# Optimization experiments

Hardware: AMD Instinct MI355X
Metric: run time of the kernel (lower is better)

The kernel has to match this reference:

```python
import jax, jax.numpy as jnp
import numpy as np

N_NODES = 1_000_000
N_EDGES = 16_000_000


def setup_inputs() -> dict:
    key = jax.random.key(0)
    k = jax.random.split(key, 6)
    x = jax.random.normal(k[0], (N_NODES, 1), dtype=jnp.float32)
    edge_index = jax.random.randint(k[1], (2, N_EDGES), 0, N_NODES, dtype=jnp.int32)
    W1 = jax.random.normal(k[2], (1, 16), dtype=jnp.float32) * (1.0 / np.sqrt(1))
    b1 = jnp.zeros((16,), dtype=jnp.float32)
    W2 = jax.random.normal(k[3], (16, 2), dtype=jnp.float32) * (1.0 / np.sqrt(16))
    b2 = jnp.zeros((2,), dtype=jnp.float32)
    return {"x": x, "edge_index": edge_index, "W1": W1, "b1": b1, "W2": W2, "b2": b2}


def _gcn_norm(edge_index, num_nodes):
    # PyG GCNConv default: add self-loops, symmetric normalization.
    loops = jnp.arange(num_nodes, dtype=edge_index.dtype)
    row = jnp.concatenate([edge_index[0], loops])  # source
    col = jnp.concatenate([edge_index[1], loops])  # target
    deg = jax.ops.segment_sum(jnp.ones_like(col, dtype=jnp.float32), col,
                              num_segments=num_nodes)
    dis = jnp.where(deg > 0, jax.lax.rsqrt(jnp.maximum(deg, 1.0)), 0.0)
    norm = dis[row] * dis[col]  # [E + N]
    return row, col, norm


def _gcn_conv(x, row, col, norm, W, b, num_nodes):
    h = x @ W                                   # [N, out]
    msg = h[row] * norm[:, None]                # gather + scale per edge
    out = jax.ops.segment_sum(msg, col, num_segments=num_nodes)
    return out + b


def reference(x, edge_index, W1, b1, W2, b2):
    n = x.shape[0]
    row, col, norm = _gcn_norm(edge_index, n)
    h = jax.nn.relu(_gcn_conv(x, row, col, norm, W1, b1, n))
    out = _gcn_conv(h, row, col, norm, W2, b2, n)
    return jax.nn.log_softmax(out, axis=1)
```

## Files before the change

kernel.cpp:

```cpp
#include <hip/hip_runtime.h>
#include <hip/hip_fp16.h>


namespace {

constexpr int N_NODES = 1000000;
constexpr int BUCKET_SHIFT = 11;
constexpr int NPB = 1 << BUCKET_SHIFT;
constexpr int NBUCKET = (N_NODES + NPB - 1) / NPB;
constexpr int CHUNK = 32768;
constexpr int NP = 512;
constexpr int TB = 1024;
constexpr int BATCH = 4096;

static_assert(NBUCKET <= 512, "wave scan assumes <=512 buckets");

typedef int intv4 __attribute__((ext_vector_type(4)));
typedef float floatv2 __attribute__((ext_vector_type(2)));

__device__ inline intv4 ntload4(const int* p) {
  return __builtin_nontemporal_load((const intv4*)p);
}
__device__ inline unsigned ntloadu(const unsigned* p) {
  return __builtin_nontemporal_load(p);
}

__device__ inline void wave_scan_512(const unsigned* arr, unsigned* outp, int n,
                                     unsigned* tot) {
  int lane = threadIdx.x;
  unsigned v[8];
  unsigned s = 0;
  int base8 = lane * 8;
#pragma unroll
  for (int k = 0; k < 8; ++k) {
    unsigned xv = (base8 + k < n) ? arr[base8 + k] : 0u;
    v[k] = s; s += xv;
  }
  unsigned run = s;
#pragma unroll
  for (int d = 1; d < 64; d <<= 1) {
    unsigned o = __shfl_up(run, d, 64);
    if (lane >= d) run += o;
  }
  unsigned excl = run - s;
#pragma unroll
  for (int k = 0; k < 8; ++k)
    if (base8 + k < n) outp[base8 + k] = excl + v[k];
  if (lane == 63 && tot) *tot = excl + s;
}


__global__ void k_hist(const int* __restrict__ col, int E,
                       unsigned* __restrict__ H) {
  __shared__ unsigned hist[NBUCKET];
  for (int i = threadIdx.x; i < NBUCKET; i += TB) hist[i] = 0u;
  __syncthreads();
  const int c = blockIdx.x;
  const int cbase = c * CHUNK;
  const int cend = min(cbase + CHUNK, E);
  for (int i0 = cbase + threadIdx.x * 4; i0 < cend; i0 += TB * 4) {
    if (i0 + 4 <= cend) {
      intv4 cc = ntload4(col + i0);
      atomicAdd(&hist[((unsigned)cc.x) >> BUCKET_SHIFT], 1u);
      atomicAdd(&hist[((unsigned)cc.y) >> BUCKET_SHIFT], 1u);
      atomicAdd(&hist[((unsigned)cc.z) >> BUCKET_SHIFT], 1u);
      atomicAdd(&hist[((unsigned)cc.w) >> BUCKET_SHIFT], 1u);
    } else {
      for (int i = i0; i < cend; ++i)
        atomicAdd(&hist[((unsigned)col[i]) >> BUCKET_SHIFT], 1u);
    }
  }
  __syncthreads();
  for (int b = threadIdx.x; b < NBUCKET; b += TB)
    H[(size_t)b * NP + c] = hist[b];
}

__global__ void k_scan1(unsigned* __restrict__ H, int nchunk,
                        unsigned* __restrict__ total) {
  unsigned* Hrow = H + (size_t)blockIdx.x * NP;
  wave_scan_512(Hrow, Hrow, nchunk, total + blockIdx.x);
}

__global__ void k_scan2(const unsigned* __restrict__ total,
                        unsigned* __restrict__ ebase) {
  wave_scan_512(total, ebase, NBUCKET, nullptr);
}

__global__ void k_bin(const int* __restrict__ row, const int* __restrict__ col,
                      int E, const unsigned* __restrict__ H,
                      const unsigned* __restrict__ ebase,
                      unsigned* __restrict__ packed) {
  __shared__ unsigned bcnt[NBUCKET];
  __shared__ unsigned boff[NBUCKET];
  __shared__ unsigned Wb[NBUCKET];
  __shared__ unsigned gcur[NBUCKET];
  __shared__ unsigned bufv[BATCH];
  __shared__ unsigned short bufb[BATCH];
  __shared__ unsigned stot;

  const int c = blockIdx.x;
  const int tid = threadIdx.x;
  for (int i = tid; i < NBUCKET; i += TB)
    gcur[i] = ebase[i] + H[(size_t)i * NP + c];
  __syncthreads();

  const int cbase = c * CHUNK;
  const int cend = min(cbase + CHUNK, E);

  for (int batch0 = cbase; batch0 < cend; batch0 += BATCH) {
    for (int i = tid; i < NBUCKET; i += TB) bcnt[i] = 0u;
    __syncthreads();

    unsigned bk[4], rk[4], pv[4];
    int nval = 0;
    const int i0 = batch0 + tid * 4;
    if (i0 + 4 <= cend) {
      intv4 cc = ntload4(col + i0);
      intv4 rr = ntload4(row + i0);
      const int ccs[4] = {cc.x, cc.y, cc.z, cc.w};
      const int rrs[4] = {rr.x, rr.y, rr.z, rr.w};
      nval = 4;
#pragma unroll
      for (int k = 0; k < 4; ++k) {
        unsigned ccv = (unsigned)ccs[k];
        bk[k] = ccv >> BUCKET_SHIFT;
        pv[k] = ((ccv & (unsigned)(NPB - 1)) << 20) | (unsigned)rrs[k];
        rk[k] = atomicAdd(&bcnt[bk[k]], 1u);
      }
    } else if (i0 < cend) {
      nval = cend - i0;
      for (int k = 0; k < nval; ++k) {
        unsigned ccv = (unsigned)col[i0 + k];
        bk[k] = ccv >> BUCKET_SHIFT;
        pv[k] = ((ccv & (unsigned)(NPB - 1)) << 20) | (unsigned)row[i0 + k];
        rk[k] = atomicAdd(&bcnt[bk[k]], 1u);
      }
    }
    __syncthreads();

    if (tid < 64) wave_scan_512(bcnt, boff, NBUCKET, &stot);
    __syncthreads();

    for (int i = tid; i < NBUCKET; i += TB) {
      Wb[i] = gcur[i] - boff[i];
      gcur[i] += bcnt[i];
    }
    __syncthreads();

    for (int k = 0; k < nval; ++k) {
      unsigned slot = boff[bk[k]] + rk[k];
      bufv[slot] = pv[k];
      bufb[slot] = (unsigned short)bk[k];
    }
    __syncthreads();

    const unsigned tot = stot;
    for (unsigned i = tid; i < tot; i += TB) {
      unsigned b = bufb[i];
      packed[Wb[b] + i] = bufv[i];
    }
    __syncthreads();
  }
}


__global__ void k_deg(const unsigned* __restrict__ packed,
                      const unsigned* __restrict__ ebase,
                      const unsigned* __restrict__ total,
                      const float* __restrict__ x,
                      float* __restrict__ dis, float* __restrict__ t) {
  __shared__ unsigned cnt[NPB];
  for (int i = threadIdx.x; i < NPB; i += TB) cnt[i] = 0u;
  __syncthreads();
  const int b = blockIdx.x;
  const unsigned e0 = ebase[b];
  const unsigned n = total[b];
#pragma unroll 4
  for (unsigned i = threadIdx.x; i < n; i += TB)
    atomicAdd(&cnt[ntloadu(packed + e0 + i) >> 20], 1u);
  __syncthreads();
  const int nodeBase = b << BUCKET_SHIFT;
  for (int i = threadIdx.x; i < NPB; i += TB) {
    int node = nodeBase + i;
    if (node < N_NODES) {
      float r = rsqrtf((float)cnt[i] + 1.0f);
      dis[node] = r;
      t[node] = x[node] * r;
    }
  }
}

__global__ void k_s(const unsigned* __restrict__ packed,
                    const unsigned* __restrict__ ebase,
                    const unsigned* __restrict__ total,
                    const float* __restrict__ dis, const float* __restrict__ t,
                    const float* __restrict__ W1, const float* __restrict__ b1,
                    const float* __restrict__ W2, __half2* __restrict__ vh) {
  __shared__ float acc[NPB];
  for (int i = threadIdx.x; i < NPB; i += TB) acc[i] = 0.f;
  __syncthreads();
  const int b = blockIdx.x;
  const unsigned e0 = ebase[b];
  const unsigned n = total[b];
#pragma unroll 4
  for (unsigned i = threadIdx.x; i < n; i += TB) {
    unsigned p = ntloadu(packed + e0 + i);
    atomicAdd(&acc[p >> 20], t[p & 0xFFFFFu]);
  }
  __syncthreads();
  const int nodeBase = b << BUCKET_SHIFT;
  for (int i = threadIdx.x; i < NPB; i += TB) {
    int node = nodeBase + i;
    if (node < N_NODES) {
      float r = dis[node];
      float s = r * (acc[i] + t[node]);
      float u0 = 0.f, u1 = 0.f;
#pragma unroll
      for (int j = 0; j < 16; ++j) {
        float h = fmaxf(fmaf(W1[j], s, b1[j]), 0.f);
        u0 = fmaf(h, W2[2 * j + 0], u0);
        u1 = fmaf(h, W2[2 * j + 1], u1);
      }
      vh[node] = __floats2half2_rn(u0 * r, u1 * r);
    }
  }
}

__global__ void k_v(const unsigned* __restrict__ packed,
                    const unsigned* __restrict__ ebase,
                    const unsigned* __restrict__ total,
                    const float* __restrict__ dis, const __half2* __restrict__ vh,
                    const float* __restrict__ b2, float* __restrict__ out) {
  __shared__ float a0[NPB];
  __shared__ float a1[NPB];
  for (int i = threadIdx.x; i < NPB; i += TB) { a0[i] = 0.f; a1[i] = 0.f; }
  __syncthreads();
  const int b = blockIdx.x;
  const unsigned e0 = ebase[b];
  const unsigned n = total[b];
#pragma unroll 4
  for (unsigned i = threadIdx.x; i < n; i += TB) {
    unsigned p = ntloadu(packed + e0 + i);
    float2 vv = __half22float2(vh[p & 0xFFFFFu]);
    unsigned l = p >> 20;
    atomicAdd(&a0[l], vv.x);
    atomicAdd(&a1[l], vv.y);
  }
  __syncthreads();
  const int nodeBase = b << BUCKET_SHIFT;
  const float bb0 = b2[0], bb1 = b2[1];
  for (int i = threadIdx.x; i < NPB; i += TB) {
    int node = nodeBase + i;
    if (node < N_NODES) {
      float r = dis[node];
      float2 vi = __half22float2(vh[node]);
      float o0 = fmaf(r, a0[i] + vi.x, bb0);
      float o1 = fmaf(r, a1[i] + vi.y, bb1);
      float m = fmaxf(o0, o1);
      float lse = m + logf(expf(o0 - m) + expf(o1 - m));
      floatv2 res;
      res.x = o0 - lse;
      res.y = o1 - lse;
      __builtin_nontemporal_store(res, (floatv2*)(out + 2 * (size_t)node));
    }
  }
}


constexpr int EDGE_GRID = 2048;
constexpr int NBS = 256;

__global__ void f_zero(float4* __restrict__ p, int n4) {
  int i = blockIdx.x * blockDim.x + threadIdx.x;
  int stride = gridDim.x * blockDim.x;
  float4 z = make_float4(0.f, 0.f, 0.f, 0.f);
  for (; i < n4; i += stride) p[i] = z;
}
__global__ void f_deg(const int4* __restrict__ col4, float* __restrict__ deg, int e4) {
  int i = blockIdx.x * blockDim.x + threadIdx.x;
  int stride = gridDim.x * blockDim.x;
  for (; i < e4; i += stride) {
    int4 c = col4[i];
    unsafeAtomicAdd(&deg[c.x], 1.0f); unsafeAtomicAdd(&deg[c.y], 1.0f);
    unsafeAtomicAdd(&deg[c.z], 1.0f); unsafeAtomicAdd(&deg[c.w], 1.0f);
  }
}
__global__ void f_node1(const float* __restrict__ x, const float* __restrict__ deg,
                        float* __restrict__ dis, float* __restrict__ t) {
  int i = blockIdx.x * blockDim.x + threadIdx.x;
  if (i >= N_NODES) return;
  float r = rsqrtf(deg[i] + 1.0f);
  dis[i] = r; t[i] = x[i] * r;
}
__global__ void f_scat_s(const int4* __restrict__ row4, const int4* __restrict__ col4,
                         const float* __restrict__ t, float* __restrict__ s_acc, int e4) {
  int i = blockIdx.x * blockDim.x + threadIdx.x;
  int stride = gridDim.x * blockDim.x;
  for (; i < e4; i += stride) {
    int4 r = row4[i]; int4 c = col4[i];
    unsafeAtomicAdd(&s_acc[c.x], t[r.x]); unsafeAtomicAdd(&s_acc[c.y], t[r.y]);
    unsafeAtomicAdd(&s_acc[c.z], t[r.z]); unsafeAtomicAdd(&s_acc[c.w], t[r.w]);
  }
}
__global__ void f_node2(const float* __restrict__ s_acc, const float* __restrict__ dis,
                        const float* __restrict__ t, const float* __restrict__ W1,
                        const float* __restrict__ b1, const float* __restrict__ W2,
                        float2* __restrict__ v) {
  int i = blockIdx.x * blockDim.x + threadIdx.x;
  if (i >= N_NODES) return;
  float r = dis[i];
  float s = r * (s_acc[i] + t[i]);
  float u0 = 0.f, u1 = 0.f;
#pragma unroll
  for (int j = 0; j < 16; ++j) {
    float h = fmaxf(fmaf(W1[j], s, b1[j]), 0.f);
    u0 = fmaf(h, W2[2 * j + 0], u0);
    u1 = fmaf(h, W2[2 * j + 1], u1);
  }
  v[i] = make_float2(u0 * r, u1 * r);
}
__global__ void f_scat_v(const int4* __restrict__ row4, const int4* __restrict__ col4,
                         const float2* __restrict__ v, float* __restrict__ acc0,
                         float* __restrict__ acc1, int e4) {
  int i = blockIdx.x * blockDim.x + threadIdx.x;
  int stride = gridDim.x * blockDim.x;
  for (; i < e4; i += stride) {
    int4 r = row4[i]; int4 c = col4[i];
    float2 v0 = v[r.x], v1 = v[r.y], v2 = v[r.z], v3 = v[r.w];
    unsafeAtomicAdd(&acc0[c.x], v0.x); unsafeAtomicAdd(&acc1[c.x], v0.y);
    unsafeAtomicAdd(&acc0[c.y], v1.x); unsafeAtomicAdd(&acc1[c.y], v1.y);
    unsafeAtomicAdd(&acc0[c.z], v2.x); unsafeAtomicAdd(&acc1[c.z], v2.y);
    unsafeAtomicAdd(&acc0[c.w], v3.x); unsafeAtomicAdd(&acc1[c.w], v3.y);
  }
}
__global__ void f_node3(const float* __restrict__ acc0, const float* __restrict__ acc1,
                        const float* __restrict__ dis, const float2* __restrict__ v,
                        const float* __restrict__ b2, float2* __restrict__ out) {
  int i = blockIdx.x * blockDim.x + threadIdx.x;
  if (i >= N_NODES) return;
  float r = dis[i];
  float2 vi = v[i];
  float o0 = fmaf(r, acc0[i] + vi.x, b2[0]);
  float o1 = fmaf(r, acc1[i] + vi.y, b2[1]);
  float m = fmaxf(o0, o1);
  float lse = m + logf(expf(o0 - m) + expf(o1 - m));
  out[i] = make_float2(o0 - lse, o1 - lse);
}

}

extern "C" void kernel_launch(void* const* d_in, const int* in_sizes, int n_in,
                              void* d_out, int out_size, void* d_ws, size_t ws_size,
                              hipStream_t stream) {
  const float* x  = (const float*)d_in[0];
  const int*   ei = (const int*)d_in[1];
  const float* W1 = (const float*)d_in[2];
  const float* b1 = (const float*)d_in[3];
  const float* W2 = (const float*)d_in[4];
  const float* b2 = (const float*)d_in[5];

  const int E = in_sizes[1] / 2;
  const int* row = ei;
  const int* col = ei + E;

  const int nchunk = (E + CHUNK - 1) / CHUNK;

  char* ws = (char*)d_ws;
  size_t off = 0;
  unsigned* packed = (unsigned*)(ws + off); off += (size_t)E * 4;
  unsigned* H      = (unsigned*)(ws + off); off += (size_t)NBUCKET * NP * 4;
  unsigned* total  = (unsigned*)(ws + off); off += 2048;
  unsigned* ebase  = (unsigned*)(ws + off); off += 2048;
  float* dis       = (float*)(ws + off);    off += (size_t)N_NODES * 4;
  float* t         = (float*)(ws + off);    off += (size_t)N_NODES * 4;
  __half2* vh      = (__half2*)(ws + off);  off += (size_t)N_NODES * 4;
  const size_t need = off;

  if (ws_size >= need && nchunk <= NP) {
    k_hist <<<nchunk, TB, 0, stream>>>(col, E, H);
    k_scan1<<<NBUCKET, 64, 0, stream>>>(H, nchunk, total);
    k_scan2<<<1, 64, 0, stream>>>(total, ebase);
    k_bin  <<<nchunk, TB, 0, stream>>>(row, col, E, H, ebase, packed);
    k_deg  <<<NBUCKET, TB, 0, stream>>>(packed, ebase, total, x, dis, t);
    k_s    <<<NBUCKET, TB, 0, stream>>>(packed, ebase, total, dis, t, W1, b1, W2, vh);
    k_v    <<<NBUCKET, TB, 0, stream>>>(packed, ebase, total, dis, vh, b2, (float*)d_out);
    return;
  }

  const int e4 = E / 4;
  float* fws   = (float*)d_ws;
  float* deg   = fws;
  float* s_acc = fws + (size_t)N_NODES;
  float* acc0  = fws + 2 * (size_t)N_NODES;
  float* acc1  = fws + 3 * (size_t)N_NODES;
  float* fdis  = fws + 4 * (size_t)N_NODES;
  float* ft    = fws + 5 * (size_t)N_NODES;
  float2* fv   = (float2*)(fws + 6 * (size_t)N_NODES);
  const int nodeGrid = (N_NODES + NBS - 1) / NBS;

  f_zero  <<<EDGE_GRID, NBS, 0, stream>>>((float4*)fws, N_NODES);
  f_deg   <<<EDGE_GRID, NBS, 0, stream>>>((const int4*)col, deg, e4);
  f_node1 <<<nodeGrid, NBS, 0, stream>>>(x, deg, fdis, ft);
  f_scat_s<<<EDGE_GRID, NBS, 0, stream>>>((const int4*)row, (const int4*)col, ft, s_acc, e4);
  f_node2 <<<nodeGrid, NBS, 0, stream>>>(s_acc, fdis, ft, W1, b1, W2, fv);
  f_scat_v<<<EDGE_GRID, NBS, 0, stream>>>((const int4*)row, (const int4*)col, fv, acc0, acc1, e4);
  f_node3 <<<nodeGrid, NBS, 0, stream>>>(acc0, acc1, fdis, fv, b2, (float2*)d_out);
}
```

Before: 554.3 us.

## Pack two fixed-point accumulators into one 64-bit LDS atomic and widen edge loads

Layer-two aggregation now converts each half2 message to biased fixed-point integers and packs both into a single 64-bit shared-memory atomicAdd, replacing two float atomics per edge. The bias is removed afterwards using the degree recovered from dis. Packed edges are also read as 64-bit pairs, with scalar head and tail handling, in the degree and both aggregation kernels. The bucketing batch doubles to eight edges per thread. The fixed-point quantization adds rounding error and depends on the bias and degree reconstruction staying within 32-bit lanes, which risks overflow or carry between the packed halves.

```diff
diff --git a/kernel.cpp b/kernel.cpp
--- a/kernel.cpp
+++ b/kernel.cpp
@@ -11,17 +11,19 @@
 constexpr int CHUNK = 32768;
 constexpr int NP = 512;
 constexpr int TB = 1024;
-constexpr int BATCH = 4096;
+constexpr int BATCH = 8192;
+
+constexpr float FPSCALE = 8192.0f;
+constexpr unsigned FPBIAS = 1u << 21;
 
 static_assert(NBUCKET <= 512, "wave scan assumes <=512 buckets");
 
 typedef int intv4 __attribute__((ext_vector_type(4)));
-typedef float floatv2 __attribute__((ext_vector_type(2)));
 
 __device__ inline intv4 ntload4(const int* p) {
   return __builtin_nontemporal_load((const intv4*)p);
 }
-__device__ inline unsigned ntloadu(const unsigned* p) {
+__device__ inline unsigned long long ntload64(const unsigned long long* p) {
   return __builtin_nontemporal_load(p);
 }
 
@@ -111,17 +113,19 @@
     for (int i = tid; i < NBUCKET; i += TB) bcnt[i] = 0u;
     __syncthreads();
 
-    unsigned bk[4], rk[4], pv[4];
+    unsigned bk[8], rk[8], pv[8];
     int nval = 0;
-    const int i0 = batch0 + tid * 4;
-    if (i0 + 4 <= cend) {
-      intv4 cc = ntload4(col + i0);
-      intv4 rr = ntload4(row + i0);
-      const int ccs[4] = {cc.x, cc.y, cc.z, cc.w};
-      const int rrs[4] = {rr.x, rr.y, rr.z, rr.w};
-      nval = 4;
-#pragma unroll
-      for (int k = 0; k < 4; ++k) {
+    const int i0 = batch0 + tid * 8;
+    if (i0 + 8 <= cend) {
+      intv4 cc0 = ntload4(col + i0);
+      intv4 cc1 = ntload4(col + i0 + 4);
+      intv4 rr0 = ntload4(row + i0);
+      intv4 rr1 = ntload4(row + i0 + 4);
+      const int ccs[8] = {cc0.x, cc0.y, cc0.z, cc0.w, cc1.x, cc1.y, cc1.z, cc1.w};
+      const int rrs[8] = {rr0.x, rr0.y, rr0.z, rr0.w, rr1.x, rr1.y, rr1.z, rr1.w};
+      nval = 8;
+#pragma unroll
+      for (int k = 0; k < 8; ++k) {
         unsigned ccv = (unsigned)ccs[k];
         bk[k] = ccv >> BUCKET_SHIFT;
         pv[k] = ((ccv & (unsigned)(NPB - 1)) << 20) | (unsigned)rrs[k];
@@ -175,9 +179,21 @@
   const int b = blockIdx.x;
   const unsigned e0 = ebase[b];
   const unsigned n = total[b];
+  const unsigned e1 = e0 + n;
+  unsigned a0 = (e0 + 1) & ~1u; if (a0 > e1) a0 = e1;
+  unsigned a1 = e1 & ~1u;       if (a1 < a0) a1 = a0;
+  if (threadIdx.x == 0) {
+    for (unsigned i = e0; i < a0; ++i) atomicAdd(&cnt[packed[i] >> 20], 1u);
+    for (unsigned i = a1; i < e1; ++i) atomicAdd(&cnt[packed[i] >> 20], 1u);
+  }
+  const unsigned npair = (a1 - a0) >> 1;
+  const unsigned long long* pp = (const unsigned long long*)(packed + a0);
 #pragma unroll 4
-  for (unsigned i = threadIdx.x; i < n; i += TB)
-    atomicAdd(&cnt[ntloadu(packed + e0 + i) >> 20], 1u);
+  for (unsigned i = threadIdx.x; i < npair; i += TB) {
+    unsigned long long w = ntload64(pp + i);
+    atomicAdd(&cnt[((unsigned)w) >> 20], 1u);
+    atomicAdd(&cnt[((unsigned)(w >> 32)) >> 20], 1u);
+  }
   __syncthreads();
   const int nodeBase = b << BUCKET_SHIFT;
   for (int i = threadIdx.x; i < NPB; i += TB) {
@@ -202,10 +218,27 @@
   const int b = blockIdx.x;
   const unsigned e0 = ebase[b];
   const unsigned n = total[b];
+  const unsigned e1 = e0 + n;
+  unsigned a0 = (e0 + 1) & ~1u; if (a0 > e1) a0 = e1;
+  unsigned a1 = e1 & ~1u;       if (a1 < a0) a1 = a0;
+  if (threadIdx.x == 0) {
+    for (unsigned i = e0; i < a0; ++i) {
+      unsigned p = packed[i];
+      atomicAdd(&acc[p >> 20], t[p & 0xFFFFFu]);
+    }
+    for (unsigned i = a1; i < e1; ++i) {
+      unsigned p = packed[i];
+      atomicAdd(&acc[p >> 20], t[p & 0xFFFFFu]);
+    }
+  }
+  const unsigned npair = (a1 - a0) >> 1;
+  const unsigned long long* pp = (const unsigned long long*)(packed + a0);
 #pragma unroll 4
-  for (unsigned i = threadIdx.x; i < n; i += TB) {
-    unsigned p = ntloadu(packed + e0 + i);
-    atomicAdd(&acc[p >> 20], t[p & 0xFFFFFu]);
+  for (unsigned i = threadIdx.x; i < npair; i += TB) {
+    unsigned long long w = ntload64(pp + i);
+    unsigned p0 = (unsigned)w, p1 = (unsigned)(w >> 32);
+    atomicAdd(&acc[p0 >> 20], t[p0 & 0xFFFFFu]);
+    atomicAdd(&acc[p1 >> 20], t[p1 & 0xFFFFFu]);
   }
   __syncthreads();
   const int nodeBase = b << BUCKET_SHIFT;
@@ -226,25 +259,39 @@
   }
 }
 
+__device__ inline void addv64(unsigned long long* a64, unsigned p,
+                              const __half2* __restrict__ vh) {
+  float2 vv = __half22float2(vh[p & 0xFFFFFu]);
+  unsigned lo = FPBIAS + (unsigned)__float2int_rn(vv.x * FPSCALE);
+  unsigned hi = FPBIAS + (unsigned)__float2int_rn(vv.y * FPSCALE);
+  atomicAdd(&a64[p >> 20], ((unsigned long long)hi << 32) | (unsigned long long)lo);
+}
+
 __global__ void k_v(const unsigned* __restrict__ packed,
                     const unsigned* __restrict__ ebase,
                     const unsigned* __restrict__ total,
                     const float* __restrict__ dis, const __half2* __restrict__ vh,
                     const float* __restrict__ b2, float* __restrict__ out) {
-  __shared__ float a0[NPB];
-  __shared__ float a1[NPB];
-  for (int i = threadIdx.x; i < NPB; i += TB) { a0[i] = 0.f; a1[i] = 0.f; }
+  __shared__ unsigned long long a64[NPB];
+  for (int i = threadIdx.x; i < NPB; i += TB) a64[i] = 0ull;
   __syncthreads();
   const int b = blockIdx.x;
   const unsigned e0 = ebase[b];
   const unsigned n = total[b];
+  const unsigned e1 = e0 + n;
+  unsigned a0 = (e0 + 1) & ~1u; if (a0 > e1) a0 = e1;
+  unsigned a1 = e1 & ~1u;       if (a1 < a0) a1 = a0;
+  if (threadIdx.x == 0) {
+    for (unsigned i = e0; i < a0; ++i) addv64(a64, packed[i], vh);
+    for (unsigned i = a1; i < e1; ++i) addv64(a64, packed[i], vh);
+  }
+  const unsigned npair = (a1 - a0) >> 1;
+  const unsigned long long* pp = (const unsigned long long*)(packed + a0);
 #pragma unroll 4
-  for (unsigned i = threadIdx.x; i < n; i += TB) {
-    unsigned p = ntloadu(packed + e0 + i);
-    float2 vv = __half22float2(vh[p & 0xFFFFFu]);
-    unsigned l = p >> 20;
-    atomicAdd(&a0[l], vv.x);
-    atomicAdd(&a1[l], vv.y);
+  for (unsigned i = threadIdx.x; i < npair; i += TB) {
+    unsigned long long w = ntload64(pp + i);
+    addv64(a64, (unsigned)w, vh);
+    addv64(a64, (unsigned)(w >> 32), vh);
   }
   __syncthreads();
   const int nodeBase = b << BUCKET_SHIFT;
@@ -253,15 +300,18 @@
     int node = nodeBase + i;
     if (node < N_NODES) {
       float r = dis[node];
+      unsigned deg = (unsigned)(roundf(1.0f / (r * r)) - 1.0f);
+      unsigned long long S = a64[i];
+      unsigned lo = (unsigned)S, hi = (unsigned)(S >> 32);
+      float s0 = (float)(int)(lo - deg * FPBIAS) * (1.0f / FPSCALE);
+      float s1 = (float)(int)(hi - deg * FPBIAS) * (1.0f / FPSCALE);
       float2 vi = __half22float2(vh[node]);
-      float o0 = fmaf(r, a0[i] + vi.x, bb0);
-      float o1 = fmaf(r, a1[i] + vi.y, bb1);
+      float o0 = fmaf(r, s0 + vi.x, bb0);
+      float o1 = fmaf(r, s1 + vi.y, bb1);
       float m = fmaxf(o0, o1);
       float lse = m + logf(expf(o0 - m) + expf(o1 - m));
-      floatv2 res;
-      res.x = o0 - lse;
-      res.y = o1 - lse;
-      __builtin_nontemporal_store(res, (floatv2*)(out + 2 * (size_t)node));
+      __builtin_nontemporal_store(o0 - lse, out + 2 * (size_t)node);
+      __builtin_nontemporal_store(o1 - lse, out + 2 * (size_t)node + 1);
     }
   }
 }
```

Result: faster. 470.7 us (-15.1%).
